# Kernel tuning notes

Hardware: AMD Instinct MI355X
Metric: run time of the kernel (lower is better)

The kernel has to match this reference:

```python
import jax, jax.numpy as jnp
import numpy as np

N_RES = 30000
N_ATOMS = 6
N_EDGES = 300000
HIDDEN = 128
N_GRAPHS = 32
CENTRAL_IDX = 1
EPS = 1e-6


def _normalize(x, axis=-1):
    # matches torch F.normalize (eps=1e-12 on the norm)
    return x / jnp.maximum(jnp.linalg.norm(x, axis=axis, keepdims=True), 1e-12)


def _rbf(D, D_min=0.0, D_max=20.0, num_rbf=16):
    mu = jnp.linspace(D_min, D_max, num_rbf)
    sigma = (D_max - D_min) / num_rbf
    return jnp.exp(-(((D[..., None] - mu) / sigma) ** 2))


def _quaternions(R):
    Rxx, Ryy, Rzz = R[:, 0, 0], R[:, 1, 1], R[:, 2, 2]
    mag = 0.5 * jnp.sqrt(jnp.abs(1.0 + jnp.stack([Rxx - Ryy - Rzz, -Rxx + Ryy - Rzz, -Rxx - Ryy + Rzz], -1)))
    signs = jnp.sign(jnp.stack([R[:, 2, 1] - R[:, 1, 2], R[:, 0, 2] - R[:, 2, 0], R[:, 1, 0] - R[:, 0, 1]], -1))
    xyz = signs * mag
    w = jnp.sqrt(jax.nn.relu(1.0 + Rxx + Ryy + Rzz))[:, None] / 2.0
    return _normalize(jnp.concatenate([xyz, w], -1))


def _layernorm(x, w, b, eps=1e-5):
    mu = x.mean(-1, keepdims=True)
    var = ((x - mu) ** 2).mean(-1, keepdims=True)
    return (x - mu) / jnp.sqrt(var + eps) * w + b


def _forward(coords, central_coords, node_W, node_b, node_ln_w, node_ln_b,
             edge_W, edge_b, edge_ln_w, edge_ln_b, batch, edge_index):
    n_res, n_atoms = coords.shape[:2]
    L = n_res * n_atoms
    src, tgt = edge_index[0], edge_index[1]

    # chain-boundary masks (replace torch's NaN-write + nan_to_num with masking to 0)
    boundary = jnp.concatenate([jnp.zeros(1, bool), batch[1:] != batch[:-1]])      # first res of new graph
    boundary_next = jnp.concatenate([boundary[1:], jnp.zeros(1, bool)])            # last res of a graph

    Xf = coords.reshape(-1, 3)
    ar = jnp.arange(L)
    col = jnp.arange(n_atoms)

    # ---- dihedral ----
    U = _normalize(Xf[1:] - Xf[:-1])
    c1 = _normalize(jnp.cross(U[:-2], U[1:-1]))
    c2 = _normalize(jnp.cross(U[1:-1], U[2:]))
    dih = jnp.arccos(jnp.clip((c1 * c2).sum(-1), -1.0 + EPS, 1.0 - EPS)) * jnp.sign((c2 * U[:-2]).sum(-1))
    dih = jnp.pad(dih, (1, 2)).reshape(n_res, n_atoms)
    d_mask = ((ar > 0) & (ar < L - 2)).reshape(n_res, n_atoms)
    d_mask = d_mask & ~(boundary[:, None] & (col == 0)[None])
    d_mask = d_mask & ~(boundary_next[:, None] & (col >= n_atoms - 2)[None])
    dih_feat = jnp.where(d_mask[..., None], jnp.stack([jnp.sin(dih), jnp.cos(dih)], -1), 0.0).reshape(n_res, -1)

    # ---- bond angle ----
    dX0 = _normalize(Xf[:-2] - Xf[1:-1])
    dX1 = _normalize(Xf[2:] - Xf[1:-1])
    cosang = (dX0 * dX1).sum(-1)
    sinang = jnp.sqrt(1.0 - cosang ** 2 + EPS)
    cosang = jnp.pad(cosang, (1, 1)).reshape(n_res, n_atoms)
    sinang = jnp.pad(sinang, (1, 1)).reshape(n_res, n_atoms)
    a_mask = ((ar > 0) & (ar < L - 1)).reshape(n_res, n_atoms)
    a_mask = a_mask & ~(boundary[:, None] & (col == 0)[None])
    a_mask = a_mask & ~(boundary_next[:, None] & (col == n_atoms - 1)[None])
    ang_feat = jnp.where(a_mask[..., None], jnp.stack([sinang, cosang], -1), 0.0).reshape(n_res, -1)

    # ---- local frame Q ----
    cX = central_coords
    du = _normalize(cX[1:] - cX[:-1])
    bvec = _normalize(du[:-1] - du[1:])
    nvec = _normalize(jnp.cross(du[:-1], du[1:]))
    Q = jnp.stack([bvec, nvec, jnp.cross(bvec, nvec)], -1)          # [n_res-2, 3, 3]
    Q = jnp.pad(Q, ((1, 1), (0, 0), (0, 0)))
    r = jnp.arange(n_res)
    q_valid = (r > 0) & (r < n_res - 1) & (~boundary) & (~boundary_next)
    Q = Q * q_valid[:, None, None]                                   # invalid frames -> 0 (== nan_to_num result)

    # ---- relative orientation quaternion per edge ----
    R = jnp.einsum('eki,ekj->eij', Q[tgt], Q[src])                   # tgt_Q^T @ src_Q
    orient = jnp.where((q_valid[src] & q_valid[tgt])[:, None], _quaternions(R), 0.0)

    # ---- inter distances / directions (edge) ----
    diff = coords[src][:, None, :, :] - coords[tgt][:, :, None, :]   # [E, n_atoms_t, n_atoms_s, 3]
    inter_D = jnp.sqrt((diff ** 2).sum(-1) + EPS)
    inter_dist = _rbf(inter_D).reshape(diff.shape[0], -1)            # [E, 576]
    inter_direct = jnp.einsum('eki,etsk->etsi', Q[tgt], _normalize(diff)).reshape(diff.shape[0], -1)  # [E, 108]

    # ---- intra distances / directions (node) ----
    keep = np.arange(n_atoms) != CENTRAL_IDX
    d_nc = coords[:, keep] - cX[:, None]                             # [n_res, 5, 3]
    intra_dist = jnp.log(jnp.sqrt((d_nc ** 2).sum(-1) + EPS))        # [n_res, 5]
    intra_direct = jnp.einsum('rki,rak->rai', Q, _normalize(d_nc)).reshape(n_res, -1)  # [n_res, 15]

    h_V = jnp.concatenate([dih_feat, ang_feat, intra_dist, intra_direct], -1)  # [n_res, 44]
    h_E = jnp.concatenate([orient, inter_dist, inter_direct], -1)              # [E, 688]
    h_V = _layernorm(h_V @ node_W + node_b, node_ln_w, node_ln_b)
    h_E = _layernorm(h_E @ edge_W + edge_b, edge_ln_w, edge_ln_b)
    return h_V, h_E


def setup_inputs() -> dict:
    key = jax.random.key(0)
    ks = jax.random.split(key, 8)
    coords = jax.random.normal(ks[0], (N_RES, N_ATOMS, 3), jnp.float32)
    central_coords = jax.random.normal(ks[1], (N_RES, 3), jnp.float32)
    batch = jnp.sort(jax.random.randint(ks[2], (N_RES,), 0, N_GRAPHS))
    edge_index = jax.random.randint(ks[3], (2, N_EDGES), 0, N_RES)
    node_W = jax.random.normal(ks[4], (44, HIDDEN), jnp.float32) / np.sqrt(44.0)
    edge_W = jax.random.normal(ks[5], (688, HIDDEN), jnp.float32) / np.sqrt(688.0)
    return {
        'coords': coords, 'central_coords': central_coords,
        'node_W': node_W, 'node_b': jnp.zeros((HIDDEN,), jnp.float32),
        'node_ln_w': jnp.ones((HIDDEN,), jnp.float32), 'node_ln_b': jnp.zeros((HIDDEN,), jnp.float32),
        'edge_W': edge_W, 'edge_b': jnp.zeros((HIDDEN,), jnp.float32),
        'edge_ln_w': jnp.ones((HIDDEN,), jnp.float32), 'edge_ln_b': jnp.zeros((HIDDEN,), jnp.float32),
        'batch': batch, 'edge_index': edge_index,
    }


def reference(coords, central_coords, node_W, node_b, node_ln_w, node_ln_b,
              edge_W, edge_b, edge_ln_w, edge_ln_b, batch, edge_index):
    return _forward(coords, central_coords, node_W, node_b, node_ln_w, node_ln_b,
                    edge_W, edge_b, edge_ln_w, edge_ln_b, batch, edge_index)
```

## Files before the change

### kernel.cpp

```cpp
#include <hip/hip_runtime.h>
#include <hip/hip_bf16.h>


#define N_RES   30000
#define N_ATOMS 6
#define LFLAT   (N_RES * N_ATOMS)
#define N_EDGES 300000
#define HID     128
#define NODE_IN 44
#define EDGE_IN 688
#define KSTEPS  43
#define KS_A    32
#define EPSF    1e-6f
#define LN_EPS  1e-5f
#define MTILE   32
#define RPB     16

typedef short short8 __attribute__((ext_vector_type(8)));
typedef float float16v __attribute__((ext_vector_type(16)));

static __device__ __forceinline__ unsigned short f2bf(float x) {
    __hip_bfloat16 h = __float2bfloat16(x);
    unsigned short u;
    __builtin_memcpy(&u, &h, 2);
    return u;
}

struct F3 { float x, y, z; };
static __device__ __forceinline__ F3 ld3(const float* p, long idx) {
    F3 r; r.x = p[idx*3+0]; r.y = p[idx*3+1]; r.z = p[idx*3+2]; return r;
}
static __device__ __forceinline__ F3 ldl(const float* p, int a) {
    F3 r; r.x = p[a*3+0]; r.y = p[a*3+1]; r.z = p[a*3+2]; return r;
}
static __device__ __forceinline__ F3 subv(F3 a, F3 b) { return {a.x-b.x, a.y-b.y, a.z-b.z}; }
static __device__ __forceinline__ float dotv(F3 a, F3 b) { return a.x*b.x + a.y*b.y + a.z*b.z; }
static __device__ __forceinline__ F3 crossv(F3 a, F3 b) {
    return {a.y*b.z - a.z*b.y, a.z*b.x - a.x*b.z, a.x*b.y - a.y*b.x};
}
static __device__ __forceinline__ F3 nrmv(F3 a) {
    float inv = rsqrtf(fmaxf(dotv(a, a), 1e-24f));
    return {a.x*inv, a.y*inv, a.z*inv};
}
static __device__ __forceinline__ float sgn(float x) { return (x > 0.f) ? 1.f : ((x < 0.f) ? -1.f : 0.f); }

__global__ void k_packw(const float* __restrict__ W, unsigned short* __restrict__ Wp) {
    int s = blockIdx.x;
    int tid = threadIdx.x;
    int w = tid >> 6, lane = tid & 63;
    int ch = w * 32 + (lane & 31);
    int kh = lane >> 5;
    uint4 out;
    uint u[4];
    #pragma unroll
    for (int jp = 0; jp < 4; ++jp) {
        unsigned int lohi[2];
        #pragma unroll
        for (int b = 0; b < 2; ++b) {
            int jj = 2 * jp + b;
            int kn = 16 * s + kh * 8 + jj;
            int ko = (kn < 684) ? (kn + 4) : (kn - 684);
            lohi[b] = f2bf(W[(long)ko * HID + ch]);
        }
        u[jp] = lohi[0] | (lohi[1] << 16);
    }
    out.x = u[0]; out.y = u[1]; out.z = u[2]; out.w = u[3];
    *(uint4*)(Wp + ((size_t)(s * 4 + w) * 64 + lane) * 8) = out;
}

__global__ void k_frames(const float* __restrict__ central, const int* __restrict__ batch,
                         float* __restrict__ Qbuf, int* __restrict__ qval) {
    int r = blockIdx.x * 256 + threadIdx.x;
    if (r >= N_RES) return;
    bool bnd   = (r > 0)         && (batch[r]   != batch[r-1]);
    bool bndn  = (r < N_RES - 1) && (batch[r+1] != batch[r]);
    bool valid = (r > 0) && (r < N_RES - 1) && !bnd && !bndn;
    float Q[9] = {0,0,0,0,0,0,0,0,0};
    if (valid) {
        F3 cp = ld3(central, (long)r-1), cc = ld3(central, (long)r), cn = ld3(central, (long)r+1);
        F3 u0 = nrmv(subv(cc, cp));
        F3 u1 = nrmv(subv(cn, cc));
        F3 b  = nrmv(subv(u0, u1));
        F3 n  = nrmv(crossv(u0, u1));
        F3 c  = crossv(b, n);
        Q[0]=b.x; Q[1]=n.x; Q[2]=c.x;
        Q[3]=b.y; Q[4]=n.y; Q[5]=c.y;
        Q[6]=b.z; Q[7]=n.z; Q[8]=c.z;
    }
    #pragma unroll
    for (int k = 0; k < 9; k++) Qbuf[(size_t)r*9 + k] = Q[k];
    qval[r] = valid ? 1 : 0;
}

__global__ __launch_bounds__(256, 4) void k_node(
    const float* __restrict__ coords, const float* __restrict__ central,
    const float* __restrict__ node_W, const float* __restrict__ node_b,
    const float* __restrict__ lnw, const float* __restrict__ lnb,
    const int* __restrict__ batch, const float* __restrict__ Qbuf,
    float* __restrict__ out) {
    __shared__ float Wlds[NODE_IN * HID];
    __shared__ float feat[RPB][NODE_IN];
    __shared__ float cst[(RPB + 2) * 18];
    __shared__ float bS[HID], lwS[HID], lbS[HID];
    __shared__ float red[8];

    int tid = threadIdx.x;
    int r0 = blockIdx.x * RPB;

    for (int i = tid; i < NODE_IN * HID; i += 256) Wlds[i] = node_W[i];
    if (tid < HID) { bS[tid] = node_b[tid]; lwS[tid] = lnw[tid]; lbS[tid] = lnb[tid]; }
    for (int i = tid; i < (RPB + 2) * 18; i += 256) {
        long g = (long)(r0 - 1) * 18 + i;
        cst[i] = (g >= 0 && g < (long)N_RES * 18) ? coords[g] : 0.f;
    }
    __syncthreads();

    if (tid < RPB * 11) {
        int rl = tid / 11, role = tid - rl * 11;
        int r = r0 + rl;
        bool bnd  = (r > 0)         && (batch[r]   != batch[r-1]);
        bool bndn = (r < N_RES - 1) && (batch[r+1] != batch[r]);
        const float* C = cst + (rl + 1) * 18;
        if (role < 6) {
            int c = role;
            long j = (long)r * N_ATOMS + c;
            float sd = 0.f, cd = 0.f;
            bool dm = (j > 0) && (j < LFLAT - 2) && !(bnd && c == 0) && !(bndn && c >= N_ATOMS - 2);
            if (dm) {
                F3 x0 = ldl(C, c-1), x1 = ldl(C, c), x2 = ldl(C, c+1), x3 = ldl(C, c+2);
                F3 u1 = nrmv(subv(x1, x0)), u2 = nrmv(subv(x2, x1)), u3 = nrmv(subv(x3, x2));
                F3 c1 = nrmv(crossv(u1, u2)), c2 = nrmv(crossv(u2, u3));
                float cc = fminf(fmaxf(dotv(c1, c2), -1.f + EPSF), 1.f - EPSF);
                float s  = sgn(dotv(c2, u1));
                sd = s * sqrtf(fmaxf(1.f - cc*cc, 0.f));
                cd = (s != 0.f) ? cc : 1.f;
            }
            feat[rl][2*c] = sd; feat[rl][2*c+1] = cd;
            float sa = 0.f, ca = 0.f;
            bool am = (j > 0) && (j < LFLAT - 1) && !(bnd && c == 0) && !(bndn && c == N_ATOMS - 1);
            if (am) {
                F3 x0 = ldl(C, c-1), x1 = ldl(C, c), x2 = ldl(C, c+1);
                F3 d0 = nrmv(subv(x0, x1)), d1 = nrmv(subv(x2, x1));
                float cv = dotv(d0, d1);
                float t = 1.f - cv*cv + EPSF;
                sa = t * rsqrtf(t);
                ca = cv;
            }
            feat[rl][12 + 2*c] = sa; feat[rl][12 + 2*c + 1] = ca;
        } else {
            int a = role - 6;
            int atom = (a == 0) ? 0 : (a + 1);
            F3 x  = ldl(C, atom);
            F3 cx = ld3(central, (long)r);
            F3 d  = subv(x, cx);
            float d2 = dotv(d, d);
            feat[rl][24 + a] = 0.5f * __logf(d2 + EPSF);
            float inv = rsqrtf(fmaxf(d2, 1e-24f));
            float nx = d.x*inv, ny = d.y*inv, nz = d.z*inv;
            const float* Q = Qbuf + (size_t)r * 9;
            #pragma unroll
            for (int i = 0; i < 3; i++)
                feat[rl][29 + a*3 + i] = Q[0+i]*nx + Q[3+i]*ny + Q[6+i]*nz;
        }
    }
    __syncthreads();

    int ch = tid & 127;
    int g  = tid >> 7;
    int w  = tid >> 6;
    for (int it = 0; it < 8; ++it) {
        int rl = it * 2 + g;
        float acc = bS[ch];
        #pragma unroll
        for (int i = 0; i < NODE_IN; i++)
            acc += feat[rl][i] * Wlds[i * HID + ch];
        float s = acc;
        #pragma unroll
        for (int m = 1; m < 64; m <<= 1) s += __shfl_xor(s, m, 64);
        if ((tid & 63) == 0) red[w] = s;
        __syncthreads();
        float mu = (red[2*g] + red[2*g+1]) * (1.f / HID);
        float dv = acc - mu;
        float q = dv * dv;
        #pragma unroll
        for (int m = 1; m < 64; m <<= 1) q += __shfl_xor(q, m, 64);
        if ((tid & 63) == 0) red[4 + w] = q;
        __syncthreads();
        float var = (red[4 + 2*g] + red[4 + 2*g + 1]) * (1.f / HID);
        out[(size_t)(r0 + rl) * HID + ch] = dv * rsqrtf(var + LN_EPS) * lwS[ch] + lbS[ch];
    }
}

__global__ __launch_bounds__(256, 4) void k_edge(
    const float* __restrict__ coords, const int* __restrict__ eidx,
    const unsigned short* __restrict__ Wpack, const float* __restrict__ edge_b,
    const float* __restrict__ lnw, const float* __restrict__ lnb,
    const float* __restrict__ Qbuf, const int* __restrict__ qval,
    float* __restrict__ outE) {
    __shared__ __align__(16) unsigned char smemA[KS_A * 64 * 8 * 2];
    __shared__ float cS[64][18];
    __shared__ float qtS[MTILE][9];
    __shared__ int sS[MTILE], tS[MTILE];

    unsigned short* Ast = (unsigned short*)smemA;
    int tid = threadIdx.x;
    int lane = tid & 63;
    int w = tid >> 6;
    int e0 = blockIdx.x * MTILE;

    if (tid < MTILE) {
        sS[tid] = eidx[e0 + tid];
        tS[tid] = eidx[N_EDGES + e0 + tid];
    }
    __syncthreads();

    #pragma unroll
    for (int it = 0; it < 5; ++it) {
        int idx = tid + it * 256;
        if (idx < 64 * 18) {
            int slot = idx / 18;
            int rem  = idx - slot * 18;
            int res  = (slot < 32) ? sS[slot] : tS[slot - 32];
            cS[slot][rem] = coords[(size_t)res * 18 + rem];
        }
    }

    uint2 qpk;
    if (tid < MTILE) {
        int s = sS[tid];
        int t = tS[tid];
        float Qs[9], Qt[9];
        #pragma unroll
        for (int k = 0; k < 9; k++) {
            Qs[k] = Qbuf[(size_t)s*9 + k];
            Qt[k] = Qbuf[(size_t)t*9 + k];
            qtS[tid][k] = Qt[k];
        }
        float R[9];
        #pragma unroll
        for (int i = 0; i < 3; i++)
            #pragma unroll
            for (int jj = 0; jj < 3; jj++)
                R[i*3+jj] = Qt[0+i]*Qs[0+jj] + Qt[3+i]*Qs[3+jj] + Qt[6+i]*Qs[6+jj];
        float m0 = 0.5f * sqrtf(fabsf(1.f + R[0] - R[4] - R[8]));
        float m1 = 0.5f * sqrtf(fabsf(1.f - R[0] + R[4] - R[8]));
        float m2 = 0.5f * sqrtf(fabsf(1.f - R[0] - R[4] + R[8]));
        float xq = sgn(R[7] - R[5]) * m0;
        float yq = sgn(R[2] - R[6]) * m1;
        float zq = sgn(R[3] - R[1]) * m2;
        float wq = 0.5f * sqrtf(fmaxf(1.f + R[0] + R[4] + R[8], 0.f));
        float inv = rsqrtf(fmaxf(xq*xq + yq*yq + zq*zq + wq*wq, 1e-24f));
        float vm = (qval[s] && qval[t]) ? 1.f : 0.f;
        qpk.x = f2bf(xq * inv * vm) | ((unsigned int)f2bf(yq * inv * vm) << 16);
        qpk.y = f2bf(zq * inv * vm) | ((unsigned int)f2bf(wq * inv * vm) << 16);
    }
    __syncthreads();

    int e  = tid & 31;
    int p0 = tid >> 5;

    #define RBF_TASK(PAIR, EV, ULO, UHI, DIR)                                        \
    {                                                                                \
        int ta = (PAIR) / 6, sa = (PAIR) - ta * 6;                                   \
        float dx = cS[EV][sa*3+0] - cS[32+(EV)][ta*3+0];                             \
        float dy = cS[EV][sa*3+1] - cS[32+(EV)][ta*3+1];                             \
        float dz = cS[EV][sa*3+2] - cS[32+(EV)][ta*3+2];                             \
        float d2 = dx*dx + dy*dy + dz*dz;                                            \
        float t  = d2 + EPSF;                                                        \
        float inv = rsqrtf(t);                                                       \
        float a8 = t * inv * 0.8f;                             \
        unsigned int uu[8];                                                          \
        _Pragma("unroll")                                                            \
        for (int i = 0; i < 8; i++) {                                                \
            float z0 = a8 - (float)(2*i)     * 1.06666672f;                          \
            float z1 = a8 - (float)(2*i + 1) * 1.06666672f;                          \
            uu[i] = f2bf(__expf(-(z0*z0))) |                                         \
                    ((unsigned int)f2bf(__expf(-(z1*z1))) << 16);                    \
        }                                                                            \
        ULO.x = uu[0]; ULO.y = uu[1]; ULO.z = uu[2]; ULO.w = uu[3];                  \
        UHI.x = uu[4]; UHI.y = uu[5]; UHI.z = uu[6]; UHI.w = uu[7];                  \
        float nx = dx*inv, ny = dy*inv, nz = dz*inv;                                 \
        _Pragma("unroll")                                                            \
        for (int i = 0; i < 3; i++)                                                  \
            DIR[i] = qtS[EV][0+i]*nx + qtS[EV][3+i]*ny + qtS[EV][6+i]*nz;            \
    }

    float vdir[4][3];
    #pragma unroll
    for (int it = 0; it < 4; ++it) {
        int pair = p0 + 8 * it;
        uint4 lo, hi;
        RBF_TASK(pair, e, lo, hi, vdir[it]);
        *(uint4*)(Ast + (pair * 64 + e) * 8)      = lo;
        *(uint4*)(Ast + (pair * 64 + 32 + e) * 8) = hi;
    }
    uint4 lo5, hi5;
    float vdir5[3];
    if (p0 < 4) {
        RBF_TASK(32 + p0, e, lo5, hi5, vdir5);
    }
    __syncthreads();

    float16v acc;
    #pragma unroll
    for (int i = 0; i < 16; i++) acc[i] = 0.f;
    const short8* Ap = (const short8*)smemA;
    const short8* Bp = (const short8*)Wpack;
    for (int s = 0; s < KS_A; ++s) {
        short8 a = Ap[s * 64 + lane];
        short8 b = Bp[(s * 4 + w) * 64 + lane];
        acc = __builtin_amdgcn_mfma_f32_32x32x16_bf16(a, b, acc, 0, 0, 0);
    }
    __syncthreads();

    if (p0 < 4) {
        *(uint4*)(Ast + (p0 * 64 + e) * 8)      = lo5;
        *(uint4*)(Ast + (p0 * 64 + 32 + e) * 8) = hi5;
        #pragma unroll
        for (int i = 0; i < 3; i++) {
            int kn = 576 + (32 + p0) * 3 + i;
            int s2 = kn >> 4, r2 = kn & 15;
            Ast[(((s2 - 32) * 64) + (r2 >> 3) * 32 + e) * 8 + (r2 & 7)] = f2bf(vdir5[i]);
        }
    }
    #pragma unroll
    for (int it = 0; it < 4; ++it) {
        int pair = p0 + 8 * it;
        #pragma unroll
        for (int i = 0; i < 3; i++) {
            int kn = 576 + pair * 3 + i;
            int s2 = kn >> 4, r2 = kn & 15;
            Ast[(((s2 - 32) * 64) + (r2 >> 3) * 32 + e) * 8 + (r2 & 7)] = f2bf(vdir[it][i]);
        }
    }
    if (tid < MTILE)
        *(uint2*)(Ast + ((10 * 64 + 32 + tid) * 8 + 4)) = qpk;
    __syncthreads();

    for (int s = KS_A; s < KSTEPS; ++s) {
        short8 a = Ap[(s - KS_A) * 64 + lane];
        short8 b = Bp[(s * 4 + w) * 64 + lane];
        acc = __builtin_amdgcn_mfma_f32_32x32x16_bf16(a, b, acc, 0, 0, 0);
    }

    __syncthreads();
    float* C_s = (float*)smemA;
    int col = lane & 31;
    #pragma unroll
    for (int r = 0; r < 16; ++r) {
        int row = (r & 3) + 8 * (r >> 2) + 4 * (lane >> 5);
        C_s[row * 132 + w * 32 + col] = acc[r];
    }
    __syncthreads();

    int ee = tid >> 3;
    int p  = tid & 7;
    const float* Crow = C_s + ee * 132 + p * 16;
    float x[16];
    float sum = 0.f;
    #pragma unroll
    for (int j = 0; j < 16; ++j) {
        x[j] = Crow[j] + edge_b[p * 16 + j];
        sum += x[j];
    }
    #pragma unroll
    for (int m = 1; m < 8; m <<= 1) sum += __shfl_xor(sum, m, 64);
    float mu = sum * (1.f / HID);
    float vs = 0.f;
    #pragma unroll
    for (int j = 0; j < 16; ++j) { float d = x[j] - mu; vs += d * d; }
    #pragma unroll
    for (int m = 1; m < 8; m <<= 1) vs += __shfl_xor(vs, m, 64);
    float is = rsqrtf(vs * (1.f / HID) + LN_EPS);
    float* op = outE + (size_t)(e0 + ee) * HID + p * 16;
    #pragma unroll
    for (int j = 0; j < 16; ++j) {
        int ch = p * 16 + j;
        op[j] = (x[j] - mu) * is * lnw[ch] + lnb[ch];
    }
}

extern "C" void kernel_launch(void* const* d_in, const int* in_sizes, int n_in,
                              void* d_out, int out_size, void* d_ws, size_t ws_size,
                              hipStream_t stream) {
    (void)in_sizes; (void)n_in; (void)out_size; (void)ws_size;
    const float* coords  = (const float*)d_in[0];
    const float* central = (const float*)d_in[1];
    const float* node_W  = (const float*)d_in[2];
    const float* node_b  = (const float*)d_in[3];
    const float* node_lw = (const float*)d_in[4];
    const float* node_lb = (const float*)d_in[5];
    const float* edge_W  = (const float*)d_in[6];
    const float* edge_b  = (const float*)d_in[7];
    const float* edge_lw = (const float*)d_in[8];
    const float* edge_lb = (const float*)d_in[9];
    const int*   batch   = (const int*)d_in[10];
    const int*   eidx    = (const int*)d_in[11];

    unsigned short* Wpack = (unsigned short*)d_ws;
    float* Qbuf = (float*)((char*)d_ws + (size_t)EDGE_IN * HID * 2);
    int*   qval = (int*)(Qbuf + (size_t)N_RES * 9);

    float* outV = (float*)d_out;
    float* outE = outV + (size_t)N_RES * HID;

    hipLaunchKernelGGL(k_packw,  dim3(KSTEPS),            dim3(256), 0, stream, edge_W, Wpack);
    hipLaunchKernelGGL(k_frames, dim3((N_RES + 255)/256), dim3(256), 0, stream, central, batch, Qbuf, qval);
    hipLaunchKernelGGL(k_node,   dim3(N_RES / RPB),       dim3(256), 0, stream,
                       coords, central, node_W, node_b, node_lw, node_lb, batch, Qbuf, outV);
    hipLaunchKernelGGL(k_edge,   dim3(N_EDGES / MTILE),   dim3(256), 0, stream,
                       coords, eidx, Wpack, edge_b, edge_lw, edge_lb, Qbuf, qval, outE);
}
```

Before: 346.6 us.

## Fuse prep kernels and merge node and edge kernels into one launch

Merges weight packing and frame computation into one prep kernel. Node and edge work now run in one main kernel, with blocks interleaved 5 edge to 1 node, so node blocks overlap with edge blocks and the separate launch tail goes away. The first MFMA K-split drops from 32 to 24 steps, which shrinks shared memory so occupancy can rise (launch bounds 5). bf16 conversion becomes a manual round-to-nearest-even bit trick. In exchange, shared memory is a union across both roles, the two block types use registers unevenly, and the phase-two A-tile layout grows.

```diff
diff --git a/kernel.cpp b/kernel.cpp
--- a/kernel.cpp
+++ b/kernel.cpp
@@ -10,20 +10,26 @@
 #define NODE_IN 44
 #define EDGE_IN 688
 #define KSTEPS  43
-#define KS_A    32
+#define KS_A    24
 #define EPSF    1e-6f
 #define LN_EPS  1e-5f
 #define MTILE   32
 #define RPB     16
+#define NEBLK   (N_EDGES / MTILE)
+#define NNBLK   (N_RES / RPB)
 
 typedef short short8 __attribute__((ext_vector_type(8)));
 typedef float float16v __attribute__((ext_vector_type(16)));
 
+static __device__ __forceinline__ unsigned int bfbits(float x) {
+    unsigned int u = __builtin_bit_cast(unsigned int, x);
+    return (u + 0x7fffu + ((u >> 16) & 1u)) >> 16;
+}
 static __device__ __forceinline__ unsigned short f2bf(float x) {
-    __hip_bfloat16 h = __float2bfloat16(x);
-    unsigned short u;
-    __builtin_memcpy(&u, &h, 2);
-    return u;
+    return (unsigned short)bfbits(x);
+}
+static __device__ __forceinline__ unsigned int pk2(float lo, float hi) {
+    return bfbits(lo) | (bfbits(hi) << 16);
 }
 
 struct F3 { float x, y, z; };
@@ -44,339 +50,346 @@
 }
 static __device__ __forceinline__ float sgn(float x) { return (x > 0.f) ? 1.f : ((x < 0.f) ? -1.f : 0.f); }
 
-__global__ void k_packw(const float* __restrict__ W, unsigned short* __restrict__ Wp) {
-    int s = blockIdx.x;
+__global__ __launch_bounds__(256) void k_prep(
+    const float* __restrict__ edge_W, const float* __restrict__ central,
+    const int* __restrict__ batch,
+    unsigned short* __restrict__ Wp, float* __restrict__ Qbuf, int* __restrict__ qval) {
+    int bid = blockIdx.x;
     int tid = threadIdx.x;
-    int w = tid >> 6, lane = tid & 63;
-    int ch = w * 32 + (lane & 31);
-    int kh = lane >> 5;
-    uint4 out;
-    uint u[4];
-    #pragma unroll
-    for (int jp = 0; jp < 4; ++jp) {
-        unsigned int lohi[2];
-        #pragma unroll
-        for (int b = 0; b < 2; ++b) {
-            int jj = 2 * jp + b;
-            int kn = 16 * s + kh * 8 + jj;
-            int ko = (kn < 684) ? (kn + 4) : (kn - 684);
-            lohi[b] = f2bf(W[(long)ko * HID + ch]);
-        }
-        u[jp] = lohi[0] | (lohi[1] << 16);
+    if (bid < KSTEPS) {
+        int s = bid;
+        int w = tid >> 6, lane = tid & 63;
+        int ch = w * 32 + (lane & 31);
+        int kh = lane >> 5;
+        uint4 out;
+        uint u[4];
+        #pragma unroll
+        for (int jp = 0; jp < 4; ++jp) {
+            int k0 = 16 * s + kh * 8 + 2 * jp;
+            int ko0 = (k0     < 684) ? (k0 + 4) : (k0 - 684);
+            int ko1 = (k0 + 1 < 684) ? (k0 + 5) : (k0 - 683);
+            u[jp] = pk2(edge_W[(long)ko0 * HID + ch], edge_W[(long)ko1 * HID + ch]);
+        }
+        out.x = u[0]; out.y = u[1]; out.z = u[2]; out.w = u[3];
+        *(uint4*)(Wp + ((size_t)(s * 4 + w) * 64 + lane) * 8) = out;
+    } else {
+        int r = (bid - KSTEPS) * 256 + tid;
+        if (r >= N_RES) return;
+        bool bnd   = (r > 0)         && (batch[r]   != batch[r-1]);
+        bool bndn  = (r < N_RES - 1) && (batch[r+1] != batch[r]);
+        bool valid = (r > 0) && (r < N_RES - 1) && !bnd && !bndn;
+        float Q[9] = {0,0,0,0,0,0,0,0,0};
+        if (valid) {
+            F3 cp = ld3(central, (long)r-1), cc = ld3(central, (long)r), cn = ld3(central, (long)r+1);
+            F3 u0 = nrmv(subv(cc, cp));
+            F3 u1 = nrmv(subv(cn, cc));
+            F3 b  = nrmv(subv(u0, u1));
+            F3 n  = nrmv(crossv(u0, u1));
+            F3 c  = crossv(b, n);
+            Q[0]=b.x; Q[1]=n.x; Q[2]=c.x;
+            Q[3]=b.y; Q[4]=n.y; Q[5]=c.y;
+            Q[6]=b.z; Q[7]=n.z; Q[8]=c.z;
+        }
+        #pragma unroll
+        for (int k = 0; k < 9; k++) Qbuf[(size_t)r*9 + k] = Q[k];
+        qval[r] = valid ? 1 : 0;
     }
-    out.x = u[0]; out.y = u[1]; out.z = u[2]; out.w = u[3];
-    *(uint4*)(Wp + ((size_t)(s * 4 + w) * 64 + lane) * 8) = out;
-}
-
-__global__ void k_frames(const float* __restrict__ central, const int* __restrict__ batch,
-                         float* __restrict__ Qbuf, int* __restrict__ qval) {
-    int r = blockIdx.x * 256 + threadIdx.x;
-    if (r >= N_RES) return;
-    bool bnd   = (r > 0)         && (batch[r]   != batch[r-1]);
-    bool bndn  = (r < N_RES - 1) && (batch[r+1] != batch[r]);
-    bool valid = (r > 0) && (r < N_RES - 1) && !bnd && !bndn;
-    float Q[9] = {0,0,0,0,0,0,0,0,0};
-    if (valid) {
-        F3 cp = ld3(central, (long)r-1), cc = ld3(central, (long)r), cn = ld3(central, (long)r+1);
-        F3 u0 = nrmv(subv(cc, cp));
-        F3 u1 = nrmv(subv(cn, cc));
-        F3 b  = nrmv(subv(u0, u1));
-        F3 n  = nrmv(crossv(u0, u1));
-        F3 c  = crossv(b, n);
-        Q[0]=b.x; Q[1]=n.x; Q[2]=c.x;
-        Q[3]=b.y; Q[4]=n.y; Q[5]=c.y;
-        Q[6]=b.z; Q[7]=n.z; Q[8]=c.z;
-    }
-    #pragma unroll
-    for (int k = 0; k < 9; k++) Qbuf[(size_t)r*9 + k] = Q[k];
-    qval[r] = valid ? 1 : 0;
-}
-
-__global__ __launch_bounds__(256, 4) void k_node(
+}
+
+__global__ __launch_bounds__(256, 5) void k_main(
     const float* __restrict__ coords, const float* __restrict__ central,
     const float* __restrict__ node_W, const float* __restrict__ node_b,
-    const float* __restrict__ lnw, const float* __restrict__ lnb,
-    const int* __restrict__ batch, const float* __restrict__ Qbuf,
-    float* __restrict__ out) {
-    __shared__ float Wlds[NODE_IN * HID];
-    __shared__ float feat[RPB][NODE_IN];
-    __shared__ float cst[(RPB + 2) * 18];
-    __shared__ float bS[HID], lwS[HID], lbS[HID];
-    __shared__ float red[8];
-
+    const float* __restrict__ node_lw, const float* __restrict__ node_lb,
+    const int* __restrict__ batch, const int* __restrict__ eidx,
+    const unsigned short* __restrict__ Wpack, const float* __restrict__ edge_b,
+    const float* __restrict__ edge_lw, const float* __restrict__ edge_lb,
+    const float* __restrict__ Qbuf, const int* __restrict__ qval,
+    float* __restrict__ outV, float* __restrict__ outE) {
+    __shared__ __align__(16) unsigned char smem[30848];
+    int bid = blockIdx.x;
+    int g = bid / 6, r6 = bid - 6 * g;
     int tid = threadIdx.x;
-    int r0 = blockIdx.x * RPB;
-
-    for (int i = tid; i < NODE_IN * HID; i += 256) Wlds[i] = node_W[i];
-    if (tid < HID) { bS[tid] = node_b[tid]; lwS[tid] = lnw[tid]; lbS[tid] = lnb[tid]; }
-    for (int i = tid; i < (RPB + 2) * 18; i += 256) {
-        long g = (long)(r0 - 1) * 18 + i;
-        cst[i] = (g >= 0 && g < (long)N_RES * 18) ? coords[g] : 0.f;
-    }
-    __syncthreads();
-
-    if (tid < RPB * 11) {
-        int rl = tid / 11, role = tid - rl * 11;
-        int r = r0 + rl;
-        bool bnd  = (r > 0)         && (batch[r]   != batch[r-1]);
-        bool bndn = (r < N_RES - 1) && (batch[r+1] != batch[r]);
-        const float* C = cst + (rl + 1) * 18;
-        if (role < 6) {
-            int c = role;
-            long j = (long)r * N_ATOMS + c;
-            float sd = 0.f, cd = 0.f;
-            bool dm = (j > 0) && (j < LFLAT - 2) && !(bnd && c == 0) && !(bndn && c >= N_ATOMS - 2);
-            if (dm) {
-                F3 x0 = ldl(C, c-1), x1 = ldl(C, c), x2 = ldl(C, c+1), x3 = ldl(C, c+2);
-                F3 u1 = nrmv(subv(x1, x0)), u2 = nrmv(subv(x2, x1)), u3 = nrmv(subv(x3, x2));
-                F3 c1 = nrmv(crossv(u1, u2)), c2 = nrmv(crossv(u2, u3));
-                float cc = fminf(fmaxf(dotv(c1, c2), -1.f + EPSF), 1.f - EPSF);
-                float s  = sgn(dotv(c2, u1));
-                sd = s * sqrtf(fmaxf(1.f - cc*cc, 0.f));
-                cd = (s != 0.f) ? cc : 1.f;
+
+    if (r6 != 5) {
+        int eb = g * 5 + r6;
+        unsigned short* Ast = (unsigned short*)smem;
+        float* cS  = (float*)(smem + 24576);
+        float* qtS = (float*)(smem + 29184);
+        int*   sS  = (int*)(smem + 30336);
+        int*   tS  = sS + MTILE;
+        int lane = tid & 63;
+        int w = tid >> 6;
+        int e0 = eb * MTILE;
+
+        if (tid < MTILE) {
+            sS[tid] = eidx[e0 + tid];
+            tS[tid] = eidx[N_EDGES + e0 + tid];
+        }
+        __syncthreads();
+
+        #pragma unroll
+        for (int it = 0; it < 5; ++it) {
+            int idx = tid + it * 256;
+            if (idx < 64 * 18) {
+                int slot = idx / 18;
+                int rem  = idx - slot * 18;
+                int res  = (slot < 32) ? sS[slot] : tS[slot - 32];
+                cS[idx] = coords[(size_t)res * 18 + rem];
             }
-            feat[rl][2*c] = sd; feat[rl][2*c+1] = cd;
-            float sa = 0.f, ca = 0.f;
-            bool am = (j > 0) && (j < LFLAT - 1) && !(bnd && c == 0) && !(bndn && c == N_ATOMS - 1);
-            if (am) {
-                F3 x0 = ldl(C, c-1), x1 = ldl(C, c), x2 = ldl(C, c+1);
-                F3 d0 = nrmv(subv(x0, x1)), d1 = nrmv(subv(x2, x1));
-                float cv = dotv(d0, d1);
-                float t = 1.f - cv*cv + EPSF;
-                sa = t * rsqrtf(t);
-                ca = cv;
+        }
+
+        uint2 qpk;
+        if (tid < MTILE) {
+            int s = sS[tid];
+            int t = tS[tid];
+            float Qs[9], Qt[9];
+            #pragma unroll
+            for (int k = 0; k < 9; k++) {
+                Qs[k] = Qbuf[(size_t)s*9 + k];
+                Qt[k] = Qbuf[(size_t)t*9 + k];
+                qtS[tid*9 + k] = Qt[k];
             }
-            feat[rl][12 + 2*c] = sa; feat[rl][12 + 2*c + 1] = ca;
-        } else {
-            int a = role - 6;
-            int atom = (a == 0) ? 0 : (a + 1);
-            F3 x  = ldl(C, atom);
-            F3 cx = ld3(central, (long)r);
-            F3 d  = subv(x, cx);
-            float d2 = dotv(d, d);
-            feat[rl][24 + a] = 0.5f * __logf(d2 + EPSF);
-            float inv = rsqrtf(fmaxf(d2, 1e-24f));
-            float nx = d.x*inv, ny = d.y*inv, nz = d.z*inv;
-            const float* Q = Qbuf + (size_t)r * 9;
+            float R[9];
             #pragma unroll
             for (int i = 0; i < 3; i++)
-                feat[rl][29 + a*3 + i] = Q[0+i]*nx + Q[3+i]*ny + Q[6+i]*nz;
-        }
-    }
-    __syncthreads();
-
-    int ch = tid & 127;
-    int g  = tid >> 7;
-    int w  = tid >> 6;
-    for (int it = 0; it < 8; ++it) {
-        int rl = it * 2 + g;
-        float acc = bS[ch];
-        #pragma unroll
-        for (int i = 0; i < NODE_IN; i++)
-            acc += feat[rl][i] * Wlds[i * HID + ch];
-        float s = acc;
-        #pragma unroll
-        for (int m = 1; m < 64; m <<= 1) s += __shfl_xor(s, m, 64);
-        if ((tid & 63) == 0) red[w] = s;
-        __syncthreads();
-        float mu = (red[2*g] + red[2*g+1]) * (1.f / HID);
-        float dv = acc - mu;
-        float q = dv * dv;
-        #pragma unroll
-        for (int m = 1; m < 64; m <<= 1) q += __shfl_xor(q, m, 64);
-        if ((tid & 63) == 0) red[4 + w] = q;
-        __syncthreads();
-        float var = (red[4 + 2*g] + red[4 + 2*g + 1]) * (1.f / HID);
-        out[(size_t)(r0 + rl) * HID + ch] = dv * rsqrtf(var + LN_EPS) * lwS[ch] + lbS[ch];
-    }
-}
-
-__global__ __launch_bounds__(256, 4) void k_edge(
-    const float* __restrict__ coords, const int* __restrict__ eidx,
-    const unsigned short* __restrict__ Wpack, const float* __restrict__ edge_b,
-    const float* __restrict__ lnw, const float* __restrict__ lnb,
-    const float* __restrict__ Qbuf, const int* __restrict__ qval,
-    float* __restrict__ outE) {
-    __shared__ __align__(16) unsigned char smemA[KS_A * 64 * 8 * 2];
-    __shared__ float cS[64][18];
-    __shared__ float qtS[MTILE][9];
-    __shared__ int sS[MTILE], tS[MTILE];
-
-    unsigned short* Ast = (unsigned short*)smemA;
-    int tid = threadIdx.x;
-    int lane = tid & 63;
-    int w = tid >> 6;
-    int e0 = blockIdx.x * MTILE;
-
-    if (tid < MTILE) {
-        sS[tid] = eidx[e0 + tid];
-        tS[tid] = eidx[N_EDGES + e0 + tid];
-    }
-    __syncthreads();
-
-    #pragma unroll
-    for (int it = 0; it < 5; ++it) {
-        int idx = tid + it * 256;
-        if (idx < 64 * 18) {
-            int slot = idx / 18;
-            int rem  = idx - slot * 18;
-            int res  = (slot < 32) ? sS[slot] : tS[slot - 32];
-            cS[slot][rem] = coords[(size_t)res * 18 + rem];
-        }
-    }
-
-    uint2 qpk;
-    if (tid < MTILE) {
-        int s = sS[tid];
-        int t = tS[tid];
-        float Qs[9], Qt[9];
-        #pragma unroll
-        for (int k = 0; k < 9; k++) {
-            Qs[k] = Qbuf[(size_t)s*9 + k];
-            Qt[k] = Qbuf[(size_t)t*9 + k];
-            qtS[tid][k] = Qt[k];
-        }
-        float R[9];
-        #pragma unroll
-        for (int i = 0; i < 3; i++)
+                #pragma unroll
+                for (int jj = 0; jj < 3; jj++)
+                    R[i*3+jj] = Qt[0+i]*Qs[0+jj] + Qt[3+i]*Qs[3+jj] + Qt[6+i]*Qs[6+jj];
+            float m0 = 0.5f * sqrtf(fabsf(1.f + R[0] - R[4] - R[8]));
+            float m1 = 0.5f * sqrtf(fabsf(1.f - R[0] + R[4] - R[8]));
+            float m2 = 0.5f * sqrtf(fabsf(1.f - R[0] - R[4] + R[8]));
+            float xq = sgn(R[7] - R[5]) * m0;
+            float yq = sgn(R[2] - R[6]) * m1;
+            float zq = sgn(R[3] - R[1]) * m2;
+            float wq = 0.5f * sqrtf(fmaxf(1.f + R[0] + R[4] + R[8], 0.f));
+            float inv = rsqrtf(fmaxf(xq*xq + yq*yq + zq*zq + wq*wq, 1e-24f));
+            float vm = (qval[s] && qval[t]) ? 1.f : 0.f;
+            qpk.x = pk2(xq * inv * vm, yq * inv * vm);
+            qpk.y = pk2(zq * inv * vm, wq * inv * vm);
+        }
+        __syncthreads();
+
+        int e  = tid & 31;
+        int p0 = tid >> 5;
+
+        #define RBF_TASK(PAIR, EV, ULO, UHI, DIR)                                        \
+        {                                                                                \
+            int ta = (PAIR) / 6, sa = (PAIR) - ta * 6;                                   \
+            const float* cs_ = cS + (EV)*18 + sa*3;                                      \
+            const float* ct_ = cS + (32+(EV))*18 + ta*3;                                 \
+            float dx = cs_[0]-ct_[0], dy = cs_[1]-ct_[1], dz = cs_[2]-ct_[2];            \
+            float d2_ = dx*dx + dy*dy + dz*dz;                                           \
+            float t_  = d2_ + EPSF;                                                      \
+            float inv_ = rsqrtf(t_);                                                     \
+            float a8 = t_ * inv_ * 0.8f;                                                 \
+            unsigned int uu[8];                                                          \
+            _Pragma("unroll")                                                            \
+            for (int i_ = 0; i_ < 8; i_++) {                                             \
+                float z0 = a8 - (float)(2*i_)     * 1.06666672f;                         \
+                float z1 = a8 - (float)(2*i_ + 1) * 1.06666672f;                         \
+                uu[i_] = pk2(__expf(-(z0*z0)), __expf(-(z1*z1)));                        \
+            }                                                                            \
+            ULO.x = uu[0]; ULO.y = uu[1]; ULO.z = uu[2]; ULO.w = uu[3];                  \
+            UHI.x = uu[4]; UHI.y = uu[5]; UHI.z = uu[6]; UHI.w = uu[7];                  \
+            float nx = dx*inv_, ny = dy*inv_, nz = dz*inv_;                              \
+            _Pragma("unroll")                                                            \
+            for (int i_ = 0; i_ < 3; i_++)                                               \
+                DIR[i_] = qtS[(EV)*9+0+i_]*nx + qtS[(EV)*9+3+i_]*ny + qtS[(EV)*9+6+i_]*nz; \
+        }
+
+        #define DIR_WRITE(PAIR, EV, DIR)                                                 \
+        {                                                                                \
+            _Pragma("unroll")                                                            \
+            for (int i_ = 0; i_ < 3; i_++) {                                             \
+                int kn = 576 + (PAIR)*3 + i_;                                            \
+                int s2 = kn >> 4, r2 = kn & 15;                                          \
+                Ast[(((s2 - KS_A)*64) + (r2>>3)*32 + (EV))*8 + (r2&7)] = f2bf(DIR[i_]);  \
+            }                                                                            \
+        }
+
+        float vdir[3][3];
+        #pragma unroll
+        for (int it = 0; it < 3; ++it) {
+            int pair = p0 + 8 * it;
+            uint4 lo, hi;
+            RBF_TASK(pair, e, lo, hi, vdir[it]);
+            *(uint4*)(Ast + (pair * 64 + e) * 8)      = lo;
+            *(uint4*)(Ast + (pair * 64 + 32 + e) * 8) = hi;
+        }
+        __syncthreads();
+
+        float16v acc;
+        #pragma unroll
+        for (int i = 0; i < 16; i++) acc[i] = 0.f;
+        const short8* Ap = (const short8*)Ast;
+        const short8* Bp = (const short8*)Wpack;
+        for (int s = 0; s < KS_A; ++s) {
+            short8 a = Ap[s * 64 + lane];
+            short8 b = Bp[(s * 4 + w) * 64 + lane];
+            acc = __builtin_amdgcn_mfma_f32_32x32x16_bf16(a, b, acc, 0, 0, 0);
+        }
+        __syncthreads();
+
+        {
+            uint4 lo, hi; float dw[3];
+            RBF_TASK(24 + p0, e, lo, hi, dw);
+            *(uint4*)(Ast + (p0 * 64 + e) * 8)      = lo;
+            *(uint4*)(Ast + (p0 * 64 + 32 + e) * 8) = hi;
+            DIR_WRITE(24 + p0, e, dw);
+        }
+        if (p0 >= 4) {
+            uint4 lo, hi; float dw[3];
+            RBF_TASK(28 + p0, e, lo, hi, dw);
+            *(uint4*)(Ast + ((4 + p0) * 64 + e) * 8)      = lo;
+            *(uint4*)(Ast + ((4 + p0) * 64 + 32 + e) * 8) = hi;
+            DIR_WRITE(28 + p0, e, dw);
+        }
+        #pragma unroll
+        for (int it = 0; it < 3; ++it)
+            DIR_WRITE(p0 + 8 * it, e, vdir[it]);
+        if (tid < MTILE)
+            *(uint2*)(Ast + ((18 * 64 + 32 + tid) * 8 + 4)) = qpk;
+        __syncthreads();
+
+        for (int s = KS_A; s < KSTEPS; ++s) {
+            short8 a = Ap[(s - KS_A) * 64 + lane];
+            short8 b = Bp[(s * 4 + w) * 64 + lane];
+            acc = __builtin_amdgcn_mfma_f32_32x32x16_bf16(a, b, acc, 0, 0, 0);
+        }
+
+        __syncthreads();
+        float* C_s = (float*)smem;
+        int col = lane & 31;
+        #pragma unroll
+        for (int r = 0; r < 16; ++r) {
+            int row = (r & 3) + 8 * (r >> 2) + 4 * (lane >> 5);
+            C_s[row * 132 + w * 32 + col] = acc[r];
+        }
+        __syncthreads();
+
+        int ee = tid >> 3;
+        int p  = tid & 7;
+        const float* Crow = C_s + ee * 132;
+        float x[16];
+        float sum = 0.f;
+        #pragma unroll
+        for (int j = 0; j < 16; ++j) {
+            int c = 8 * j + p;
+            x[j] = Crow[c] + edge_b[c];
+            sum += x[j];
+        }
+        #pragma unroll
+        for (int m = 1; m < 8; m <<= 1) sum += __shfl_xor(sum, m, 64);
+        float mu = sum * (1.f / HID);
+        float vs = 0.f;
+        #pragma unroll
+        for (int j = 0; j < 16; ++j) { float d = x[j] - mu; vs += d * d; }
+        #pragma unroll
+        for (int m = 1; m < 8; m <<= 1) vs += __shfl_xor(vs, m, 64);
+        float is = rsqrtf(vs * (1.f / HID) + LN_EPS);
+        float* op = outE + (size_t)(e0 + ee) * HID;
+        #pragma unroll
+        for (int j = 0; j < 16; ++j) {
+            int c = 8 * j + p;
+            op[c] = (x[j] - mu) * is * edge_lw[c] + edge_lb[c];
+        }
+        #undef RBF_TASK
+        #undef DIR_WRITE
+    } else {
+        int nb = g;
+        float* Wlds = (float*)smem;
+        float* feat = (float*)(smem + 22528);
+        float* cst  = (float*)(smem + 25344);
+        float* bS   = (float*)(smem + 26640);
+        float* lwS  = (float*)(smem + 27152);
+        float* lbS  = (float*)(smem + 27664);
+        float* red  = (float*)(smem + 28176);
+        int r0 = nb * RPB;
+
+        const float4* W4 = (const float4*)node_W;
+        float4* Wl4 = (float4*)Wlds;
+        for (int i = tid; i < NODE_IN * HID / 4; i += 256) Wl4[i] = W4[i];
+        if (tid < HID) { bS[tid] = node_b[tid]; lwS[tid] = node_lw[tid]; lbS[tid] = node_lb[tid]; }
+        for (int i = tid; i < (RPB + 2) * 18; i += 256) {
+            long gg = (long)(r0 - 1) * 18 + i;
+            cst[i] = (gg >= 0 && gg < (long)N_RES * 18) ? coords[gg] : 0.f;
+        }
+        __syncthreads();
+
+        if (tid < RPB * 11) {
+            int rl = tid / 11, role = tid - rl * 11;
+            int r = r0 + rl;
+            bool bnd  = (r > 0)         && (batch[r]   != batch[r-1]);
+            bool bndn = (r < N_RES - 1) && (batch[r+1] != batch[r]);
+            const float* C = cst + (rl + 1) * 18;
+            if (role < 6) {
+                int c = role;
+                long j = (long)r * N_ATOMS + c;
+                float sd = 0.f, cd = 0.f;
+                bool dm = (j > 0) && (j < LFLAT - 2) && !(bnd && c == 0) && !(bndn && c >= N_ATOMS - 2);
+                if (dm) {
+                    F3 x0 = ldl(C, c-1), x1 = ldl(C, c), x2 = ldl(C, c+1), x3 = ldl(C, c+2);
+                    F3 u1 = nrmv(subv(x1, x0)), u2 = nrmv(subv(x2, x1)), u3 = nrmv(subv(x3, x2));
+                    F3 c1 = nrmv(crossv(u1, u2)), c2 = nrmv(crossv(u2, u3));
+                    float cc = fminf(fmaxf(dotv(c1, c2), -1.f + EPSF), 1.f - EPSF);
+                    float s  = sgn(dotv(c2, u1));
+                    sd = s * sqrtf(fmaxf(1.f - cc*cc, 0.f));
+                    cd = (s != 0.f) ? cc : 1.f;
+                }
+                feat[rl*NODE_IN + 2*c] = sd; feat[rl*NODE_IN + 2*c+1] = cd;
+                float sa = 0.f, ca = 0.f;
+                bool am = (j > 0) && (j < LFLAT - 1) && !(bnd && c == 0) && !(bndn && c == N_ATOMS - 1);
+                if (am) {
+                    F3 x0 = ldl(C, c-1), x1 = ldl(C, c), x2 = ldl(C, c+1);
+                    F3 d0 = nrmv(subv(x0, x1)), d1 = nrmv(subv(x2, x1));
+                    float cv = dotv(d0, d1);
+                    float t = 1.f - cv*cv + EPSF;
+                    sa = t * rsqrtf(t);
+                    ca = cv;
+                }
+                feat[rl*NODE_IN + 12 + 2*c] = sa; feat[rl*NODE_IN + 12 + 2*c + 1] = ca;
+            } else {
+                int a = role - 6;
+                int atom = (a == 0) ? 0 : (a + 1);
+                F3 x  = ldl(C, atom);
+                F3 cx = ld3(central, (long)r);
+                F3 d  = subv(x, cx);
+                float d2 = dotv(d, d);
+                feat[rl*NODE_IN + 24 + a] = 0.5f * __logf(d2 + EPSF);
+                float inv = rsqrtf(fmaxf(d2, 1e-24f));
+                float nx = d.x*inv, ny = d.y*inv, nz = d.z*inv;
+                const float* Q = Qbuf + (size_t)r * 9;
+                #pragma unroll
+                for (int i = 0; i < 3; i++)
+                    feat[rl*NODE_IN + 29 + a*3 + i] = Q[0+i]*nx + Q[3+i]*ny + Q[6+i]*nz;
+            }
+        }
+        __syncthreads();
+
+        int ch = tid & 127;
+        int sg = tid >> 7;
+        int w  = tid >> 6;
+        for (int it = 0; it < 8; ++it) {
+            int rl = it * 2 + sg;
+            float acc = bS[ch];
             #pragma unroll
-            for (int jj = 0; jj < 3; jj++)
-                R[i*3+jj] = Qt[0+i]*Qs[0+jj] + Qt[3+i]*Qs[3+jj] + Qt[6+i]*Qs[6+jj];
-        float m0 = 0.5f * sqrtf(fabsf(1.f + R[0] - R[4] - R[8]));
-        float m1 = 0.5f * sqrtf(fabsf(1.f - R[0] + R[4] - R[8]));
-        float m2 = 0.5f * sqrtf(fabsf(1.f - R[0] - R[4] + R[8]));
-        float xq = sgn(R[7] - R[5]) * m0;
-        float yq = sgn(R[2] - R[6]) * m1;
-        float zq = sgn(R[3] - R[1]) * m2;
-        float wq = 0.5f * sqrtf(fmaxf(1.f + R[0] + R[4] + R[8], 0.f));
-        float inv = rsqrtf(fmaxf(xq*xq + yq*yq + zq*zq + wq*wq, 1e-24f));
-        float vm = (qval[s] && qval[t]) ? 1.f : 0.f;
-        qpk.x = f2bf(xq * inv * vm) | ((unsigned int)f2bf(yq * inv * vm) << 16);
-        qpk.y = f2bf(zq * inv * vm) | ((unsigned int)f2bf(wq * inv * vm) << 16);
-    }
-    __syncthreads();
-
-    int e  = tid & 31;
-    int p0 = tid >> 5;
-
-    #define RBF_TASK(PAIR, EV, ULO, UHI, DIR)                                        \
-    {                                                                                \
-        int ta = (PAIR) / 6, sa = (PAIR) - ta * 6;                                   \
-        float dx = cS[EV][sa*3+0] - cS[32+(EV)][ta*3+0];                             \
-        float dy = cS[EV][sa*3+1] - cS[32+(EV)][ta*3+1];                             \
-        float dz = cS[EV][sa*3+2] - cS[32+(EV)][ta*3+2];                             \
-        float d2 = dx*dx + dy*dy + dz*dz;                                            \
-        float t  = d2 + EPSF;                                                        \
-        float inv = rsqrtf(t);                                                       \
-        float a8 = t * inv * 0.8f;                             \
-        unsigned int uu[8];                                                          \
-        _Pragma("unroll")                                                            \
-        for (int i = 0; i < 8; i++) {                                                \
-            float z0 = a8 - (float)(2*i)     * 1.06666672f;                          \
-            float z1 = a8 - (float)(2*i + 1) * 1.06666672f;                          \
-            uu[i] = f2bf(__expf(-(z0*z0))) |                                         \
-                    ((unsigned int)f2bf(__expf(-(z1*z1))) << 16);                    \
-        }                                                                            \
-        ULO.x = uu[0]; ULO.y = uu[1]; ULO.z = uu[2]; ULO.w = uu[3];                  \
-        UHI.x = uu[4]; UHI.y = uu[5]; UHI.z = uu[6]; UHI.w = uu[7];                  \
-        float nx = dx*inv, ny = dy*inv, nz = dz*inv;                                 \
-        _Pragma("unroll")                                                            \
-        for (int i = 0; i < 3; i++)                                                  \
-            DIR[i] = qtS[EV][0+i]*nx + qtS[EV][3+i]*ny + qtS[EV][6+i]*nz;            \
-    }
-
-    float vdir[4][3];
-    #pragma unroll
-    for (int it = 0; it < 4; ++it) {
-        int pair = p0 + 8 * it;
-        uint4 lo, hi;
-        RBF_TASK(pair, e, lo, hi, vdir[it]);
-        *(uint4*)(Ast + (pair * 64 + e) * 8)      = lo;
-        *(uint4*)(Ast + (pair * 64 + 32 + e) * 8) = hi;
-    }
-    uint4 lo5, hi5;
-    float vdir5[3];
-    if (p0 < 4) {
-        RBF_TASK(32 + p0, e, lo5, hi5, vdir5);
-    }
-    __syncthreads();
-
-    float16v acc;
-    #pragma unroll
-    for (int i = 0; i < 16; i++) acc[i] = 0.f;
-    const short8* Ap = (const short8*)smemA;
-    const short8* Bp = (const short8*)Wpack;
-    for (int s = 0; s < KS_A; ++s) {
-        short8 a = Ap[s * 64 + lane];
-        short8 b = Bp[(s * 4 + w) * 64 + lane];
-        acc = __builtin_amdgcn_mfma_f32_32x32x16_bf16(a, b, acc, 0, 0, 0);
-    }
-    __syncthreads();
-
-    if (p0 < 4) {
-        *(uint4*)(Ast + (p0 * 64 + e) * 8)      = lo5;
-        *(uint4*)(Ast + (p0 * 64 + 32 + e) * 8) = hi5;
-        #pragma unroll
-        for (int i = 0; i < 3; i++) {
-            int kn = 576 + (32 + p0) * 3 + i;
-            int s2 = kn >> 4, r2 = kn & 15;
-            Ast[(((s2 - 32) * 64) + (r2 >> 3) * 32 + e) * 8 + (r2 & 7)] = f2bf(vdir5[i]);
-        }
-    }
-    #pragma unroll
-    for (int it = 0; it < 4; ++it) {
-        int pair = p0 + 8 * it;
-        #pragma unroll
-        for (int i = 0; i < 3; i++) {
-            int kn = 576 + pair * 3 + i;
-            int s2 = kn >> 4, r2 = kn & 15;
-            Ast[(((s2 - 32) * 64) + (r2 >> 3) * 32 + e) * 8 + (r2 & 7)] = f2bf(vdir[it][i]);
-        }
-    }
-    if (tid < MTILE)
-        *(uint2*)(Ast + ((10 * 64 + 32 + tid) * 8 + 4)) = qpk;
-    __syncthreads();
-
-    for (int s = KS_A; s < KSTEPS; ++s) {
-        short8 a = Ap[(s - KS_A) * 64 + lane];
-        short8 b = Bp[(s * 4 + w) * 64 + lane];
-        acc = __builtin_amdgcn_mfma_f32_32x32x16_bf16(a, b, acc, 0, 0, 0);
-    }
-
-    __syncthreads();
-    float* C_s = (float*)smemA;
-    int col = lane & 31;
-    #pragma unroll
-    for (int r = 0; r < 16; ++r) {
-        int row = (r & 3) + 8 * (r >> 2) + 4 * (lane >> 5);
-        C_s[row * 132 + w * 32 + col] = acc[r];
-    }
-    __syncthreads();
-
-    int ee = tid >> 3;
-    int p  = tid & 7;
-    const float* Crow = C_s + ee * 132 + p * 16;
-    float x[16];
-    float sum = 0.f;
-    #pragma unroll
-    for (int j = 0; j < 16; ++j) {
-        x[j] = Crow[j] + edge_b[p * 16 + j];
-        sum += x[j];
-    }
-    #pragma unroll
-    for (int m = 1; m < 8; m <<= 1) sum += __shfl_xor(sum, m, 64);
-    float mu = sum * (1.f / HID);
-    float vs = 0.f;
-    #pragma unroll
-    for (int j = 0; j < 16; ++j) { float d = x[j] - mu; vs += d * d; }
-    #pragma unroll
-    for (int m = 1; m < 8; m <<= 1) vs += __shfl_xor(vs, m, 64);
-    float is = rsqrtf(vs * (1.f / HID) + LN_EPS);
-    float* op = outE + (size_t)(e0 + ee) * HID + p * 16;
-    #pragma unroll
-    for (int j = 0; j < 16; ++j) {
-        int ch = p * 16 + j;
-        op[j] = (x[j] - mu) * is * lnw[ch] + lnb[ch];
+            for (int i = 0; i < NODE_IN; i++)
+                acc += feat[rl*NODE_IN + i] * Wlds[i * HID + ch];
+            float s = acc;
+            #pragma unroll
+            for (int m = 1; m < 64; m <<= 1) s += __shfl_xor(s, m, 64);
+            if ((tid & 63) == 0) red[w] = s;
+            __syncthreads();
+            float mu = (red[2*sg] + red[2*sg+1]) * (1.f / HID);
+            float dv = acc - mu;
+            float q = dv * dv;
+            #pragma unroll
+            for (int m = 1; m < 64; m <<= 1) q += __shfl_xor(q, m, 64);
+            if ((tid & 63) == 0) red[4 + w] = q;
+            __syncthreads();
+            float var = (red[4 + 2*sg] + red[4 + 2*sg + 1]) * (1.f / HID);
+            outV[(size_t)(r0 + rl) * HID + ch] = dv * rsqrtf(var + LN_EPS) * lwS[ch] + lbS[ch];
+        }
     }
 }
 
@@ -404,10 +417,9 @@
     float* outV = (float*)d_out;
     float* outE = outV + (size_t)N_RES * HID;
 
-    hipLaunchKernelGGL(k_packw,  dim3(KSTEPS),            dim3(256), 0, stream, edge_W, Wpack);
-    hipLaunchKernelGGL(k_frames, dim3((N_RES + 255)/256), dim3(256), 0, stream, central, batch, Qbuf, qval);
-    hipLaunchKernelGGL(k_node,   dim3(N_RES / RPB),       dim3(256), 0, stream,
-                       coords, central, node_W, node_b, node_lw, node_lb, batch, Qbuf, outV);
-    hipLaunchKernelGGL(k_edge,   dim3(N_EDGES / MTILE),   dim3(256), 0, stream,
-                       coords, eidx, Wpack, edge_b, edge_lw, edge_lb, Qbuf, qval, outE);
-}
+    hipLaunchKernelGGL(k_prep, dim3(KSTEPS + (N_RES + 255) / 256), dim3(256), 0, stream,
+                       edge_W, central, batch, Wpack, Qbuf, qval);
+    hipLaunchKernelGGL(k_main, dim3(NEBLK + NNBLK), dim3(256), 0, stream,
+                       coords, central, node_W, node_b, node_lw, node_lb, batch, eidx,
+                       Wpack, edge_b, edge_lw, edge_lb, Qbuf, qval, outV, outE);
+}
```

Measured after the change: 348.0 us. Within noise of the previous version (+0.4%).
